# Optimization experiments

Measured on AMD Instinct MI355X. Metric: run time of the kernel, lower is better.

Reference implementation:

```python
import jax, jax.numpy as jnp
import numpy as np

L, E, H, FFE = 4, 512, 8, 512  # layers, embed, heads, ff dim (must equal E for residual)
HD = E // H


def _ln(x, g, b):
    mu = jnp.mean(x, -1, keepdims=True)
    var = jnp.mean((x - mu) ** 2, -1, keepdims=True)
    return (x - mu) / jnp.sqrt(var + 1e-5) * g + b


def setup_inputs() -> dict:
    key = jax.random.key(0)
    ks = jax.random.split(key, 8)
    B, S = 8, 128
    w = lambda k, shape: jax.random.normal(k, shape, jnp.float32) * 0.02
    return {
        "x": jax.random.normal(ks[0], (B, S, E), jnp.float32),
        "Wq": w(ks[1], (L, E, E)), "bq": jnp.zeros((L, E), jnp.float32),
        "Wk": w(ks[2], (L, E, E)), "bk": jnp.zeros((L, E), jnp.float32),
        "Wv": w(ks[3], (L, E, E)), "bv": jnp.zeros((L, E), jnp.float32),
        "Wo": w(ks[4], (L, E, E)), "bo": jnp.zeros((L, E), jnp.float32),
        "Wf": w(ks[5], (L, E, FFE)), "bf": jnp.zeros((L, FFE), jnp.float32),
        "g1": jnp.ones((L, E), jnp.float32), "b1": jnp.zeros((L, E), jnp.float32),
        "g2": jnp.ones((L, FFE), jnp.float32), "b2": jnp.zeros((L, FFE), jnp.float32),
    }


def reference(x, Wq, bq, Wk, bk, Wv, bv, Wo, bo, Wf, bf, g1, b1, g2, b2):
    B, S, _ = x.shape

    def stack(xb, mask):
        # xb: [B,S,E]; mask: [S] bool, True = key position inside current prefix.
        # Non-causal MHA restricted to prefix keys exactly reproduces running
        # the original stack on x[:, :s, :] (query positions beyond the prefix
        # produce values we never read).
        h = xb
        for l in range(L):
            q = (h @ Wq[l] + bq[l]).reshape(B, S, H, HD)
            k = (h @ Wk[l] + bk[l]).reshape(B, S, H, HD)
            v = (h @ Wv[l] + bv[l]).reshape(B, S, H, HD)
            sc = jnp.einsum('bqhd,bkhd->bhqk', q, k) / jnp.sqrt(jnp.float32(HD))
            sc = jnp.where(mask[None, None, None, :], sc, jnp.float32(-1e9))
            a = jax.nn.softmax(sc, axis=-1)
            o = jnp.einsum('bhqk,bkhd->bqhd', a, v).reshape(B, S, E)
            h = _ln(o @ Wo[l] + bo[l] + h, g1[l], b1[l])          # MHA + residual + LN1
            h = _ln(jax.nn.relu(h @ Wf[l] + bf[l]) + h, g2[l], b2[l])  # FF + ReLU + residual + LN2
        return h

    # masks[s-1] selects keys 0..s-1 -> prefix of length s
    masks = jnp.tril(jnp.ones((S, S), bool))
    outs = jax.vmap(stack, in_axes=(None, 0))(x, masks)  # [S, B, S, E]
    idx = jnp.arange(S)
    last = outs[idx, :, idx]  # [S, B, E]: last valid token of each prefix run
    return jnp.transpose(last, (1, 0, 2))  # [B, S, E]
```

## Files before the change

kernel.cpp:

```cpp
#include <hip/hip_runtime.h>
#include <stdint.h>

typedef unsigned short u16;
typedef __attribute__((ext_vector_type(8))) short bf16x8;
typedef __attribute__((ext_vector_type(4))) float f32x4;

#define EE 512
#define NH 8
#define HDm 64
#define SS 128
#define NB 8
#define NL 4
#define QKVW 1536

__device__ __forceinline__ float bf2f(u16 v){ union{uint32_t u; float f;} c; c.u=((uint32_t)v)<<16; return c.f; }
__device__ __forceinline__ u16 f2bf(float f){ union{float f; uint32_t u;} c; c.f=f; uint32_t u=c.u; return (u16)((u + 0x7FFFu + ((u>>16)&1u))>>16); }

__device__ __forceinline__ f32x4 mfma16(bf16x8 a, bf16x8 b, f32x4 c){
  return __builtin_amdgcn_mfma_f32_16x16x32_bf16(a,b,c,0,0,0);
}

__device__ __forceinline__ void gload16(const u16* g, u16* l){
  auto gp = reinterpret_cast<const __attribute__((address_space(1))) uint32_t*>(reinterpret_cast<uintptr_t>(g));
  auto lp = reinterpret_cast<__attribute__((address_space(3))) uint32_t*>(reinterpret_cast<uintptr_t>(l));
  __builtin_amdgcn_global_load_lds(gp, lp, 16, 0, 0);
}

#define ABAR() asm volatile("s_barrier" ::: "memory")
#define SB0()  __builtin_amdgcn_sched_barrier(0)

__device__ __forceinline__ void run_map(int bid, int cb, int U, int& r, int& u){
  int rr = 0;
  for (;;){
    int g = (cb + rr) >> 4;
    int gend = ((g + 1) << 4) - cb;
    int upr = (g + 1) * U;
    int span = (gend - rr) * upr;
    if (bid < span){ r = rr + bid / upr; u = bid % upr; return; }
    bid -= span; rr = gend;
  }
}

__global__ __launch_bounds__(256) void wtransT(const float* __restrict__ W, u16* __restrict__ dst,
                                               int dstL, int dstOff){
  __shared__ float tl[32][33];
  int l = blockIdx.y;
  int tile = blockIdx.x;
  int ot = tile & 15, it = tile >> 4;
  int t = threadIdx.x;
  int c = t & 31, r = t >> 5;
  #pragma unroll
  for (int k=0;k<4;k++){
    int ri = it*32 + r + k*8;
    tl[c][r + k*8] = W[(size_t)l*262144 + (size_t)ri*512 + ot*32 + c];
  }
  __syncthreads();
  #pragma unroll
  for (int k=0;k<4;k++){
    int ro = ot*32 + r + k*8;
    dst[(size_t)l*dstL + (size_t)(dstOff + ro)*512 + it*32 + c] = f2bf(tl[r + k*8][c]);
  }
}

__global__ __launch_bounds__(256) void bfuse(const float* __restrict__ bq, const float* __restrict__ bk,
                                             const float* __restrict__ bv, float* __restrict__ bqkv){
  int i = blockIdx.x*256 + threadIdx.x;
  int l = i / QKVW, n = i % QKVW;
  const float* b = (n < 512) ? bq : ((n < 1024) ? bk : bv);
  bqkv[i] = b[l*EE + (n & 511)];
}

__global__ __launch_bounds__(256) void hinit(const float* __restrict__ x, u16* __restrict__ h0){
  int i = (blockIdx.x*256 + threadIdx.x)*8;
  int e = i & 511;
  int pb = i >> 9;
  int b = pb & 7, pp = pb >> 3;
  const float* xp = x + (((size_t)b*SS + pp)<<9) + e;
  union{ bf16x8 v; u16 u[8]; } r;
  #pragma unroll
  for (int j=0;j<8;j++) r.u[j] = f2bf(xp[j]);
  *(bf16x8*)(h0 + i) = r.v;
}

template<int MODE>
__global__ __launch_bounds__(256) void gemm_bt(const u16* __restrict__ A, const u16* __restrict__ Bt,
                                               const float* __restrict__ bias, const u16* __restrict__ res,
                                               u16* __restrict__ o0, u16* __restrict__ o1, u16* __restrict__ o2,
                                               int cb, size_t res_mask){
  __shared__ u16 As[2][128*32];
  __shared__ u16 Bs[2][128*32];
  int t = threadIdx.x;
  size_t m0;
  if (cb < 0){
    m0 = (size_t)blockIdx.x * 128;
  } else {
    int r, tile; run_map(blockIdx.x, cb, 1, r, tile);
    m0 = (size_t)r*1024 + (size_t)tile*128;
  }
  int n0 = blockIdx.y*128;
  int wid=t>>6, lane=t&63;
  int wm=wid>>1, wn=wid&1, lr=lane&15, lk=(lane>>4)*8;
  f32x4 acc[4][4] = {};
  int srow=t>>2, scol=(t&3)*8;
  const u16* gA = A + (m0+(size_t)srow)*EE + scol;
  const u16* gB = Bt + ((size_t)(n0+srow))*EE + scol;

  auto stage = [&](int kt, int slot){
    int k0 = kt*32;
    u16* lA = As[slot] + t*8;
    u16* lB = Bs[slot] + t*8;
    gload16(gA+k0, lA);
    gload16(gA+64*EE+k0, lA+2048);
    gload16(gB+k0, lB);
    gload16(gB+64*EE+k0, lB+2048);
  };

  stage(0,0); stage(1,1);

  #pragma unroll
  for (int kt=0; kt<16; kt++){
    int slot = kt & 1;
    if (kt < 15) asm volatile("s_waitcnt vmcnt(4)" ::: "memory");
    else         asm volatile("s_waitcnt vmcnt(0)" ::: "memory");
    ABAR();
    bf16x8 a[4], b[4];
    #pragma unroll
    for (int mi=0;mi<4;mi++) a[mi] = *(const bf16x8*)(As[slot] + (wm*64+mi*16+lr)*32 + lk);
    #pragma unroll
    for (int ni=0;ni<4;ni++) b[ni] = *(const bf16x8*)(Bs[slot] + (wn*64+ni*16+lr)*32 + lk);
    asm volatile("s_waitcnt lgkmcnt(0)" ::: "memory");
    SB0();
    ABAR();
    if (kt < 14) stage(kt+2, slot);
    #pragma unroll
    for (int mi=0;mi<4;mi++)
      #pragma unroll
      for (int ni=0;ni<4;ni++)
        acc[mi][ni] = mfma16(a[mi], b[ni], acc[mi][ni]);
  }

  int g4 = lane>>4;
  u16* outp;
  int nb;
  if (MODE==0){ int sel = n0 >> 9; outp = sel==0 ? o0 : (sel==1 ? o1 : o2); nb = n0 & 511; }
  else        { outp = o0; nb = n0; }
  #pragma unroll
  for (int ni=0;ni<4;ni++){
    int coln = wn*64 + ni*16 + lr;
    float bv = bias[n0 + coln];
    int col = nb + coln;
    #pragma unroll
    for (int mi=0;mi<4;mi++){
      #pragma unroll
      for (int j=0;j<4;j++){
        size_t row = m0 + (size_t)(wm*64 + mi*16 + g4*4 + j);
        float v = acc[mi][ni][j] + bv;
        if (MODE==2) v = fmaxf(v, 0.f);
        if (MODE>=1) v += bf2f(res[(row & res_mask)*EE + col]);
        outp[row*EE + col] = f2bf(v);
      }
    }
  }
}

__global__ __launch_bounds__(256) void attn(const u16* __restrict__ Q, const u16* __restrict__ K,
                                            const u16* __restrict__ V, u16* __restrict__ Oq,
                                            int cb, int shared_qkv){
  __shared__ u16 Ks[128*72];
  __shared__ u16 Vt[64*136];
  __shared__ u16 Ps[4][16*136];
  int t = threadIdx.x;
  int idx = blockIdx.x;
  int hh = idx & 7, b = (idx>>3)&7, r = idx>>6;
  int m_run = cb + r;
  const size_t RS = (size_t)SS*NB*EE;
  size_t rbase = shared_qkv ? 0 : (size_t)r*RS;
  size_t hb = (size_t)b*EE + hh*HDm;
  size_t obase = (size_t)r*RS + hb;
  int nkc = m_run/32 + 1;
  int nkt = nkc*2;
  int nqt = m_run/16 + 1;
  int nkr = nkt*16;
  for (int i=t; i<nkr*8; i+=256){
    int row=i>>3, c=(i&7)*8;
    *(uint4*)(Ks + row*72 + c) = *(const uint4*)(K + rbase + (size_t)row*NB*EE + hb + c);
  }
  for (int i=t; i<nkr*8; i+=256){
    int row=i>>3, c=(i&7)*8;
    uint4 raw = *(const uint4*)(V + rbase + (size_t)row*NB*EE + hb + c);
    const u16* pv = (const u16*)&raw;
    #pragma unroll
    for (int j=0;j<8;j++) Vt[(c+j)*136 + row] = pv[j];
  }
  __syncthreads();
  int wid=t>>6, lane=t&63, lr=lane&15, g=lane>>4, lk=(lane>>4)*8;
  u16* Pw = Ps[wid];
  for (int iq=0; iq<2; iq++){
    int qt = wid*2 + iq;
    if (qt >= nqt) continue;
    const u16* qrow = Q + rbase + (size_t)(qt*16+lr)*NB*EE + hb;
    bf16x8 qa0 = *(const bf16x8*)(qrow + lk);
    bf16x8 qa1 = *(const bf16x8*)(qrow + 32 + lk);
    f32x4 sc[8];
    #pragma unroll
    for (int kt=0;kt<8;kt++){
      if (kt < nkt){
        f32x4 c = {};
        bf16x8 kb0 = *(const bf16x8*)(Ks + (kt*16+lr)*72 + lk);
        bf16x8 kb1 = *(const bf16x8*)(Ks + (kt*16+lr)*72 + 32 + lk);
        c = mfma16(qa0, kb0, c);
        c = mfma16(qa1, kb1, c);
        int key = kt*16 + lr;
        #pragma unroll
        for (int i2=0;i2<4;i2++)
          sc[kt][i2] = (key <= m_run) ? c[i2]*0.125f : -1e9f;
      }
    }
    #pragma unroll
    for (int i2=0;i2<4;i2++){
      float v = -3.0e38f;
      #pragma unroll
      for (int kt=0;kt<8;kt++) if (kt<nkt) v = fmaxf(v, sc[kt][i2]);
      v = fmaxf(v, __shfl_xor(v,1));
      v = fmaxf(v, __shfl_xor(v,2));
      v = fmaxf(v, __shfl_xor(v,4));
      v = fmaxf(v, __shfl_xor(v,8));
      float s = 0.f;
      #pragma unroll
      for (int kt=0;kt<8;kt++) if (kt<nkt){ float e2=__expf(sc[kt][i2]-v); sc[kt][i2]=e2; s+=e2; }
      s += __shfl_xor(s,1); s += __shfl_xor(s,2); s += __shfl_xor(s,4); s += __shfl_xor(s,8);
      float inv = 1.f/s;
      #pragma unroll
      for (int kt=0;kt<8;kt++) if (kt<nkt) sc[kt][i2] *= inv;
    }
    #pragma unroll
    for (int kt=0;kt<8;kt++) if (kt<nkt){
      #pragma unroll
      for (int i2=0;i2<4;i2++)
        Pw[(g*4+i2)*136 + kt*16 + lr] = f2bf(sc[kt][i2]);
    }
    f32x4 oa[4] = {};
    #pragma unroll
    for (int kc=0;kc<4;kc++) if (kc<nkc){
      bf16x8 pa = *(const bf16x8*)(Pw + lr*136 + kc*32 + lk);
      #pragma unroll
      for (int dt=0;dt<4;dt++){
        bf16x8 vb = *(const bf16x8*)(Vt + (dt*16+lr)*136 + kc*32 + lk);
        oa[dt] = mfma16(pa, vb, oa[dt]);
      }
    }
    #pragma unroll
    for (int dt=0;dt<4;dt++){
      #pragma unroll
      for (int j=0;j<4;j++){
        size_t prow = (size_t)(qt*16 + g*4 + j);
        Oq[obase + prow*NB*EE + dt*16 + lr] = f2bf(oa[dt][j]);
      }
    }
  }
}

__global__ __launch_bounds__(256) void lnorm(const u16* __restrict__ in, const float* __restrict__ gg,
                                             const float* __restrict__ bb, u16* __restrict__ outp, int cb){
  int r, u; run_map(blockIdx.x, cb, 32, r, u);
  size_t row = (size_t)r*1024 + (size_t)u*4 + (threadIdx.x>>6);
  int lane = threadIdx.x & 63;
  const u16* p = in + row*EE + lane*8;
  union{ bf16x8 v; u16 u[8]; } d; d.v = *(const bf16x8*)p;
  float f[8]; float s=0.f;
  #pragma unroll
  for (int j=0;j<8;j++){ f[j]=bf2f(d.u[j]); s+=f[j]; }
  #pragma unroll
  for (int o=1;o<64;o<<=1) s += __shfl_xor(s,o);
  float mu = s*(1.f/512.f);
  float s2=0.f;
  #pragma unroll
  for (int j=0;j<8;j++){ float tt=f[j]-mu; s2+=tt*tt; }
  #pragma unroll
  for (int o=1;o<64;o<<=1) s2 += __shfl_xor(s2,o);
  float rstd = rsqrtf(s2*(1.f/512.f)+1e-5f);
  union{ bf16x8 v; u16 u[8]; } rr;
  #pragma unroll
  for (int j=0;j<8;j++) rr.u[j] = f2bf((f[j]-mu)*rstd*gg[lane*8+j] + bb[lane*8+j]);
  *(bf16x8*)(outp + row*EE + lane*8) = rr.v;
}

__global__ __launch_bounds__(256) void extract(const u16* __restrict__ h, float* __restrict__ out, int cb){
  int i = blockIdx.x*256 + threadIdx.x;
  int e = i & 511;
  int b = (i >> 9) & 7;
  int r = i >> 12;
  int m = cb + r;
  out[((size_t)b*SS + m)*EE + e] = bf2f(h[(((size_t)r*SS + m)*NB + b)*EE + e]);
}

extern "C" void kernel_launch(void* const* d_in, const int* in_sizes, int n_in,
                              void* d_out, int out_size, void* d_ws, size_t ws_size,
                              hipStream_t stream){
  const float* x   = (const float*)d_in[0];
  const float* Wq  = (const float*)d_in[1];
  const float* bq  = (const float*)d_in[2];
  const float* Wk  = (const float*)d_in[3];
  const float* bk  = (const float*)d_in[4];
  const float* Wv  = (const float*)d_in[5];
  const float* bv  = (const float*)d_in[6];
  const float* Wo  = (const float*)d_in[7];
  const float* bo  = (const float*)d_in[8];
  const float* Wf  = (const float*)d_in[9];
  const float* bfb = (const float*)d_in[10];
  const float* g1  = (const float*)d_in[11];
  const float* b1  = (const float*)d_in[12];
  const float* g2  = (const float*)d_in[13];
  const float* b2  = (const float*)d_in[14];
  float* out = (float*)d_out;

  uint8_t* p = (uint8_t*)d_ws;
  u16* WqkvT = (u16*)p; p += (size_t)NL*QKVW*EE*2;
  u16* WoT   = (u16*)p; p += (size_t)NL*EE*EE*2;
  u16* WfT   = (u16*)p; p += (size_t)NL*EE*EE*2;
  float* bqkv= (float*)p; p += (size_t)NL*QKVW*4;
  u16* h0    = (u16*)p; p += (size_t)SS*NB*EE*2;
  u16* q0    = (u16*)p; p += (size_t)SS*NB*EE*2;
  u16* k0    = (u16*)p; p += (size_t)SS*NB*EE*2;
  u16* v0    = (u16*)p; p += (size_t)SS*NB*EE*2;
  size_t used = (size_t)(p - (uint8_t*)d_ws);

  int RC = 128;
  const size_t PER_RUN = (size_t)SS*NB*EE*2*5;
  while (RC > 1 && used + (size_t)RC*PER_RUN > ws_size) RC >>= 1;

  const size_t BUF = (size_t)RC*SS*NB*EE*2;
  u16* h   = (u16*)p; p += BUF;
  u16* q   = (u16*)p; p += BUF;
  u16* k   = (u16*)p; p += BUF;
  u16* v   = (u16*)p; p += BUF;
  u16* tmp = (u16*)p; p += BUF;

  const size_t NOMASK = ~(size_t)0;
  const int QL = QKVW*EE;
  const int OL = EE*EE;

  wtransT<<<dim3(256,NL),256,0,stream>>>(Wq, WqkvT, QL, 0);
  wtransT<<<dim3(256,NL),256,0,stream>>>(Wk, WqkvT, QL, 512);
  wtransT<<<dim3(256,NL),256,0,stream>>>(Wv, WqkvT, QL, 1024);
  wtransT<<<dim3(256,NL),256,0,stream>>>(Wo, WoT, OL, 0);
  wtransT<<<dim3(256,NL),256,0,stream>>>(Wf, WfT, OL, 0);
  bfuse<<<24,256,0,stream>>>(bq, bk, bv, bqkv);
  hinit<<<256,256,0,stream>>>(x, h0);
  gemm_bt<0><<<dim3(8,12),256,0,stream>>>(h0, WqkvT, bqkv, nullptr, q0, k0, v0, -1, 0);

  for (int cb=0; cb<SS; cb+=RC){
    int t128 = 0;
    for (int r2=0;r2<RC;r2++) t128 += (cb+r2)/16 + 1;

    attn<<<dim3(RC*64),256,0,stream>>>(q0, k0, v0, q, cb, 1);
    gemm_bt<1><<<dim3(t128,4),256,0,stream>>>(q, WoT, bo, h0, tmp, tmp, tmp, cb, (size_t)1023);
    lnorm<<<dim3(t128*32),256,0,stream>>>(tmp, g1, b1, h, cb);
    gemm_bt<2><<<dim3(t128,4),256,0,stream>>>(h, WfT, bfb, h, tmp, tmp, tmp, cb, NOMASK);
    lnorm<<<dim3(t128*32),256,0,stream>>>(tmp, g2, b2, h, cb);

    for (int l=1;l<NL;l++){
      gemm_bt<0><<<dim3(t128,12),256,0,stream>>>(h, WqkvT+(size_t)l*QL, bqkv+l*QKVW, nullptr, q, k, v, cb, 0);
      attn<<<dim3(RC*64),256,0,stream>>>(q, k, v, q, cb, 0);
      gemm_bt<1><<<dim3(t128,4),256,0,stream>>>(q, WoT+(size_t)l*OL, bo+l*EE, h, tmp, tmp, tmp, cb, NOMASK);
      lnorm<<<dim3(t128*32),256,0,stream>>>(tmp, g1+l*EE, b1+l*EE, h, cb);
      gemm_bt<2><<<dim3(t128,4),256,0,stream>>>(h, WfT+(size_t)l*OL, bfb+l*EE, h, tmp, tmp, tmp, cb, NOMASK);
      lnorm<<<dim3(t128*32),256,0,stream>>>(tmp, g2+l*EE, b2+l*EE, h, cb);
    }
    extract<<<dim3(RC*16),256,0,stream>>>(h, out, cb);
  }
}
```

Measured before the change: 1.976 ms.

## Double GEMM K-tile to 64 with XOR-swizzled LDS layout, halve run chunk

```diff
diff --git a/kernel.cpp b/kernel.cpp
--- a/kernel.cpp
+++ b/kernel.cpp
@@ -87,8 +87,8 @@
                                                const float* __restrict__ bias, const u16* __restrict__ res,
                                                u16* __restrict__ o0, u16* __restrict__ o1, u16* __restrict__ o2,
                                                int cb, size_t res_mask){
-  __shared__ u16 As[2][128*32];
-  __shared__ u16 Bs[2][128*32];
+  __shared__ u16 As[2][128*64];
+  __shared__ u16 Bs[2][128*64];
   int t = threadIdx.x;
   size_t m0;
   if (cb < 0){
@@ -99,44 +99,62 @@
   }
   int n0 = blockIdx.y*128;
   int wid=t>>6, lane=t&63;
-  int wm=wid>>1, wn=wid&1, lr=lane&15, lk=(lane>>4)*8;
+  int wm=wid>>1, wn=wid&1, lr=lane&15, lq=lane>>4;
   f32x4 acc[4][4] = {};
-  int srow=t>>2, scol=(t&3)*8;
-  const u16* gA = A + (m0+(size_t)srow)*EE + scol;
-  const u16* gB = Bt + ((size_t)(n0+srow))*EE + scol;
+  int srow = t>>3;
+  int cg = (t&7) ^ (srow&7);
+  const u16* gA = A + (m0+(size_t)srow)*EE + cg*8;
+  const u16* gB = Bt + ((size_t)(n0+srow))*EE + cg*8;
 
   auto stage = [&](int kt, int slot){
-    int k0 = kt*32;
+    int k0 = kt*64;
     u16* lA = As[slot] + t*8;
     u16* lB = Bs[slot] + t*8;
-    gload16(gA+k0, lA);
-    gload16(gA+64*EE+k0, lA+2048);
-    gload16(gB+k0, lB);
-    gload16(gB+64*EE+k0, lB+2048);
+    #pragma unroll
+    for (int j=0;j<4;j++){
+      gload16(gA + (size_t)j*32*EE + k0, lA + j*2048);
+      gload16(gB + (size_t)j*32*EE + k0, lB + j*2048);
+    }
   };
 
   stage(0,0); stage(1,1);
 
   #pragma unroll
-  for (int kt=0; kt<16; kt++){
+  for (int kt=0; kt<8; kt++){
     int slot = kt & 1;
-    if (kt < 15) asm volatile("s_waitcnt vmcnt(4)" ::: "memory");
-    else         asm volatile("s_waitcnt vmcnt(0)" ::: "memory");
+    if (kt < 7) asm volatile("s_waitcnt vmcnt(8)" ::: "memory");
+    else        asm volatile("s_waitcnt vmcnt(0)" ::: "memory");
     ABAR();
-    bf16x8 a[4], b[4];
-    #pragma unroll
-    for (int mi=0;mi<4;mi++) a[mi] = *(const bf16x8*)(As[slot] + (wm*64+mi*16+lr)*32 + lk);
-    #pragma unroll
-    for (int ni=0;ni<4;ni++) b[ni] = *(const bf16x8*)(Bs[slot] + (wn*64+ni*16+lr)*32 + lk);
+    bf16x8 a[4][2], b[4][2];
+    #pragma unroll
+    for (int mi=0;mi<4;mi++){
+      int row = wm*64 + mi*16 + lr;
+      #pragma unroll
+      for (int kk=0;kk<2;kk++){
+        int c = (kk*4 + lq) ^ (row&7);
+        a[mi][kk] = *(const bf16x8*)(As[slot] + row*64 + c*8);
+      }
+    }
+    #pragma unroll
+    for (int ni=0;ni<4;ni++){
+      int row = wn*64 + ni*16 + lr;
+      #pragma unroll
+      for (int kk=0;kk<2;kk++){
+        int c = (kk*4 + lq) ^ (row&7);
+        b[ni][kk] = *(const bf16x8*)(Bs[slot] + row*64 + c*8);
+      }
+    }
     asm volatile("s_waitcnt lgkmcnt(0)" ::: "memory");
     SB0();
     ABAR();
-    if (kt < 14) stage(kt+2, slot);
+    if (kt < 6) stage(kt+2, slot);
     #pragma unroll
     for (int mi=0;mi<4;mi++)
       #pragma unroll
-      for (int ni=0;ni<4;ni++)
-        acc[mi][ni] = mfma16(a[mi], b[ni], acc[mi][ni]);
+      for (int ni=0;ni<4;ni++){
+        acc[mi][ni] = mfma16(a[mi][0], b[ni][0], acc[mi][ni]);
+        acc[mi][ni] = mfma16(a[mi][1], b[ni][1], acc[mi][ni]);
+      }
   }
 
   int g4 = lane>>4;
@@ -325,7 +343,7 @@
   u16* v0    = (u16*)p; p += (size_t)SS*NB*EE*2;
   size_t used = (size_t)(p - (uint8_t*)d_ws);
 
-  int RC = 128;
+  int RC = 64;
   const size_t PER_RUN = (size_t)SS*NB*EE*2*5;
   while (RC > 1 && used + (size_t)RC*PER_RUN > ws_size) RC >>= 1;
 
```

After: 1.945 ms. About the same (-1.6%).

## Fold LayerNorm into GEMM epilogues via row statistics and pre-scaled weights

Applied to the files above, without the earlier changes.

```diff
diff --git a/kernel.cpp b/kernel.cpp
--- a/kernel.cpp
+++ b/kernel.cpp
@@ -42,7 +42,7 @@
 }
 
 __global__ __launch_bounds__(256) void wtransT(const float* __restrict__ W, u16* __restrict__ dst,
-                                               int dstL, int dstOff){
+                                               int dstL, int dstOff, const float* __restrict__ sv, int smode){
   __shared__ float tl[32][33];
   int l = blockIdx.y;
   int tile = blockIdx.x;
@@ -55,10 +55,13 @@
     tl[c][r + k*8] = W[(size_t)l*262144 + (size_t)ri*512 + ot*32 + c];
   }
   __syncthreads();
+  float sc = 1.f;
+  if (smode == 1) sc = sv[l*512 + it*32 + c];
+  else if (smode == 2) sc = (l == 0) ? 1.f : sv[(l-1)*512 + it*32 + c];
   #pragma unroll
   for (int k=0;k<4;k++){
     int ro = ot*32 + r + k*8;
-    dst[(size_t)l*dstL + (size_t)(dstOff + ro)*512 + it*32 + c] = f2bf(tl[r + k*8][c]);
+    dst[(size_t)l*dstL + (size_t)(dstOff + ro)*512 + it*32 + c] = f2bf(tl[r + k*8][c] * sc);
   }
 }
 
@@ -68,6 +71,29 @@
   int l = i / QKVW, n = i % QKVW;
   const float* b = (n < 512) ? bq : ((n < 1024) ? bk : bv);
   bqkv[i] = b[l*EE + (n & 511)];
+}
+
+__global__ __launch_bounds__(256) void gbcomp(const u16* __restrict__ WT, long wtStrideL, int wtOff,
+                                              const float* __restrict__ Wf, const float* __restrict__ bvv,
+                                              int lw0, int lg0, int Lcount,
+                                              float2* __restrict__ outGB, int outStrideL, int outOff){
+  int cidx = blockIdx.x*4 + (threadIdx.x>>6);
+  if (cidx >= Lcount*512) return;
+  int idx = cidx>>9, n = cidx&511;
+  int lane = threadIdx.x & 63;
+  const u16* wt = WT + (size_t)(lw0+idx)*wtStrideL + ((size_t)(wtOff+n))*512 + lane*8;
+  bf16x8 wv = *(const bf16x8*)wt;
+  const float* wsrc = Wf + (size_t)(lw0+idx)*262144 + ((size_t)(lane*8))*512 + n;
+  const float* bp = bvv + (lg0+idx)*512 + lane*8;
+  float gs = 0.f, bs = 0.f;
+  #pragma unroll
+  for (int j=0;j<8;j++){
+    gs += bf2f(((const u16*)&wv)[j]);
+    bs += bp[j]*wsrc[(size_t)j*512];
+  }
+  #pragma unroll
+  for (int o=1;o<64;o<<=1){ gs += __shfl_xor(gs,o); bs += __shfl_xor(bs,o); }
+  if (lane == 0) outGB[idx*outStrideL + outOff + n] = make_float2(gs, bs);
 }
 
 __global__ __launch_bounds__(256) void hinit(const float* __restrict__ x, u16* __restrict__ h0){
@@ -82,11 +108,18 @@
   *(bf16x8*)(h0 + i) = r.v;
 }
 
-template<int MODE>
-__global__ __launch_bounds__(256) void gemm_bt(const u16* __restrict__ A, const u16* __restrict__ Bt,
-                                               const float* __restrict__ bias, const u16* __restrict__ res,
-                                               u16* __restrict__ o0, u16* __restrict__ o1, u16* __restrict__ o2,
-                                               int cb, size_t res_mask){
+template<int EPI, int RESMODE>
+__global__ __launch_bounds__(256) void gemm_bt(const u16* A, const u16* Bt,
+                                               const float* __restrict__ bias,
+                                               const float2* __restrict__ GB,
+                                               const float2* statsA,
+                                               const u16* resb,
+                                               const float2* statsR,
+                                               const float* __restrict__ resG, const float* __restrict__ resB,
+                                               size_t res_mask,
+                                               u16* o0, u16* o1, u16* o2,
+                                               float2* statsOut,
+                                               int cb){
   __shared__ u16 As[2][128*32];
   __shared__ u16 Bs[2][128*32];
   int t = threadIdx.x;
@@ -140,25 +173,89 @@
   }
 
   int g4 = lane>>4;
-  u16* outp;
-  int nb;
-  if (MODE==0){ int sel = n0 >> 9; outp = sel==0 ? o0 : (sel==1 ? o1 : o2); nb = n0 & 511; }
-  else        { outp = o0; nb = n0; }
+  float mu_[4][4] = {}, rs_[4][4] = {};
+  if (EPI==0 || EPI==2 || (EPI==1 && RESMODE==1)){
+    const float2* stp = (EPI==1) ? statsR : statsA;
+    #pragma unroll
+    for (int mi=0;mi<4;mi++){
+      #pragma unroll
+      for (int j=0;j<4;j++){
+        size_t row = m0 + (size_t)(wm*64 + mi*16 + g4*4 + j);
+        float s=0.f, qq=0.f;
+        #pragma unroll
+        for (int k2=0;k2<8;k2++){ float2 e = stp[row*8 + k2]; s += e.x; qq += e.y; }
+        float mu = s*(1.f/512.f);
+        float var = qq*(1.f/512.f) - mu*mu;
+        mu_[mi][j] = mu;
+        rs_[mi][j] = rsqrtf(var + 1e-5f);
+      }
+    }
+  }
+  f32x4 psum[4] = {}, psq[4] = {};
+  u16* outp; int nb;
+  if (EPI==0 || EPI==3){ int sel = n0 >> 9; outp = sel==0 ? o0 : (sel==1 ? o1 : o2); nb = n0 & 511; }
+  else                 { outp = o0; nb = n0; }
   #pragma unroll
   for (int ni=0;ni<4;ni++){
     int coln = wn*64 + ni*16 + lr;
-    float bv = bias[n0 + coln];
-    int col = nb + coln;
+    int gcol = n0 + coln;
+    int col  = nb + coln;
+    float bv = bias[gcol];
+    float gw = 0.f, bw = 0.f, rg = 0.f, rb2 = 0.f;
+    if (EPI==0 || EPI==2){ float2 gbv = GB[(EPI==0) ? gcol : col]; gw = gbv.x; bw = gbv.y; }
+    if ((EPI==1 && RESMODE==1) || EPI==2){ rg = resG[col]; rb2 = resB[col]; }
     #pragma unroll
     for (int mi=0;mi<4;mi++){
       #pragma unroll
       for (int j=0;j<4;j++){
         size_t row = m0 + (size_t)(wm*64 + mi*16 + g4*4 + j);
-        float v = acc[mi][ni][j] + bv;
-        if (MODE==2) v = fmaxf(v, 0.f);
-        if (MODE>=1) v += bf2f(res[(row & res_mask)*EE + col]);
+        float sacc = acc[mi][ni][j];
+        float v;
+        if (EPI==3){
+          v = sacc + bv;
+        } else if (EPI==0){
+          float mu = mu_[mi][j], rs = rs_[mi][j];
+          v = rs*sacc - mu*rs*gw + bw + bv;
+        } else if (EPI==1){
+          float rv;
+          if (RESMODE==0) rv = bf2f(resb[(row & res_mask)*EE + col]);
+          else {
+            float mu = mu_[mi][j], rs = rs_[mi][j];
+            rv = (bf2f(resb[row*EE + col]) - mu)*rs*rg + rb2;
+          }
+          v = sacc + bv + rv;
+        } else {
+          float mu = mu_[mi][j], rs = rs_[mi][j];
+          float u = rs*sacc - mu*rs*gw + bw + bv;
+          u = fmaxf(u, 0.f);
+          float rv = (bf2f(resb[row*EE + col]) - mu)*rs*rg + rb2;
+          v = u + rv;
+        }
         outp[row*EE + col] = f2bf(v);
+        if (EPI==1 || EPI==2){ psum[mi][j] += v; psq[mi][j] += v*v; }
       }
+    }
+  }
+  if (EPI==1 || EPI==2){
+    #pragma unroll
+    for (int o=1;o<16;o<<=1){
+      #pragma unroll
+      for (int mi=0;mi<4;mi++)
+        #pragma unroll
+        for (int j=0;j<4;j++){
+          psum[mi][j] += __shfl_xor(psum[mi][j], o);
+          psq[mi][j]  += __shfl_xor(psq[mi][j], o);
+        }
+    }
+    if (lr == 0){
+      int slot = blockIdx.y*2 + wn;
+      #pragma unroll
+      for (int mi=0;mi<4;mi++)
+        #pragma unroll
+        for (int j=0;j<4;j++){
+          size_t row = m0 + (size_t)(wm*64 + mi*16 + g4*4 + j);
+          statsOut[row*8 + slot] = make_float2(psum[mi][j], psq[mi][j]);
+        }
     }
   }
 }
@@ -260,38 +357,31 @@
   }
 }
 
-__global__ __launch_bounds__(256) void lnorm(const u16* __restrict__ in, const float* __restrict__ gg,
-                                             const float* __restrict__ bb, u16* __restrict__ outp, int cb){
-  int r, u; run_map(blockIdx.x, cb, 32, r, u);
-  size_t row = (size_t)r*1024 + (size_t)u*4 + (threadIdx.x>>6);
-  int lane = threadIdx.x & 63;
-  const u16* p = in + row*EE + lane*8;
-  union{ bf16x8 v; u16 u[8]; } d; d.v = *(const bf16x8*)p;
-  float f[8]; float s=0.f;
-  #pragma unroll
-  for (int j=0;j<8;j++){ f[j]=bf2f(d.u[j]); s+=f[j]; }
-  #pragma unroll
-  for (int o=1;o<64;o<<=1) s += __shfl_xor(s,o);
-  float mu = s*(1.f/512.f);
-  float s2=0.f;
-  #pragma unroll
-  for (int j=0;j<8;j++){ float tt=f[j]-mu; s2+=tt*tt; }
-  #pragma unroll
-  for (int o=1;o<64;o<<=1) s2 += __shfl_xor(s2,o);
-  float rstd = rsqrtf(s2*(1.f/512.f)+1e-5f);
-  union{ bf16x8 v; u16 u[8]; } rr;
-  #pragma unroll
-  for (int j=0;j<8;j++) rr.u[j] = f2bf((f[j]-mu)*rstd*gg[lane*8+j] + bb[lane*8+j]);
-  *(bf16x8*)(outp + row*EE + lane*8) = rr.v;
-}
-
-__global__ __launch_bounds__(256) void extract(const u16* __restrict__ h, float* __restrict__ out, int cb){
-  int i = blockIdx.x*256 + threadIdx.x;
-  int e = i & 511;
-  int b = (i >> 9) & 7;
-  int r = i >> 12;
+__global__ __launch_bounds__(256) void extractLN(const u16* __restrict__ hr2, const float2* __restrict__ stats2,
+                                                 const float* __restrict__ g, const float* __restrict__ b,
+                                                 float* __restrict__ out, int cb){
+  int r = blockIdx.x;
+  int t = threadIdx.x;
   int m = cb + r;
-  out[((size_t)b*SS + m)*EE + e] = bf2f(h[(((size_t)r*SS + m)*NB + b)*EE + e]);
+  #pragma unroll
+  for (int it=0; it<2; it++){
+    int chunk = it*256 + t;
+    int b3 = chunk >> 6;
+    int e0 = (chunk & 63)*8;
+    size_t row = ((size_t)r*SS + m)*NB + b3;
+    float s=0.f, qq=0.f;
+    #pragma unroll
+    for (int k2=0;k2<8;k2++){ float2 e = stats2[row*8 + k2]; s += e.x; qq += e.y; }
+    float mu = s*(1.f/512.f);
+    float var = qq*(1.f/512.f) - mu*mu;
+    float rs = rsqrtf(var + 1e-5f);
+    bf16x8 hv = *(const bf16x8*)(hr2 + row*EE + e0);
+    #pragma unroll
+    for (int j2=0;j2<8;j2++){
+      float v = (bf2f(((const u16*)&hv)[j2]) - mu)*rs*g[e0+j2] + b[e0+j2];
+      out[((size_t)b3*SS + m)*EE + e0 + j2] = v;
+    }
+  }
 }
 
 extern "C" void kernel_launch(void* const* d_in, const int* in_sizes, int n_in,
@@ -315,58 +405,76 @@
   float* out = (float*)d_out;
 
   uint8_t* p = (uint8_t*)d_ws;
-  u16* WqkvT = (u16*)p; p += (size_t)NL*QKVW*EE*2;
-  u16* WoT   = (u16*)p; p += (size_t)NL*EE*EE*2;
-  u16* WfT   = (u16*)p; p += (size_t)NL*EE*EE*2;
-  float* bqkv= (float*)p; p += (size_t)NL*QKVW*4;
-  u16* h0    = (u16*)p; p += (size_t)SS*NB*EE*2;
-  u16* q0    = (u16*)p; p += (size_t)SS*NB*EE*2;
-  u16* k0    = (u16*)p; p += (size_t)SS*NB*EE*2;
-  u16* v0    = (u16*)p; p += (size_t)SS*NB*EE*2;
+  u16* WqkvT  = (u16*)p; p += (size_t)NL*QKVW*EE*2;
+  u16* WoT    = (u16*)p; p += (size_t)NL*EE*EE*2;
+  u16* WfT    = (u16*)p; p += (size_t)NL*EE*EE*2;
+  float* bqkv = (float*)p; p += (size_t)NL*QKVW*4;
+  float2* GBqkv = (float2*)p; p += (size_t)3*QKVW*8;
+  float2* GBf   = (float2*)p; p += (size_t)NL*EE*8;
+  u16* h0 = (u16*)p; p += (size_t)SS*NB*EE*2;
+  u16* q0 = (u16*)p; p += (size_t)SS*NB*EE*2;
+  u16* k0 = (u16*)p; p += (size_t)SS*NB*EE*2;
+  u16* v0 = (u16*)p; p += (size_t)SS*NB*EE*2;
   size_t used = (size_t)(p - (uint8_t*)d_ws);
 
   int RC = 128;
-  const size_t PER_RUN = (size_t)SS*NB*EE*2*5;
+  const size_t PER_RUN = (size_t)SS*NB*EE*2*5 + (size_t)SS*NB*8*8*2;
   while (RC > 1 && used + (size_t)RC*PER_RUN > ws_size) RC >>= 1;
 
   const size_t BUF = (size_t)RC*SS*NB*EE*2;
-  u16* h   = (u16*)p; p += BUF;
+  u16* hr1 = (u16*)p; p += BUF;
+  u16* hr2 = (u16*)p; p += BUF;
   u16* q   = (u16*)p; p += BUF;
   u16* k   = (u16*)p; p += BUF;
   u16* v   = (u16*)p; p += BUF;
-  u16* tmp = (u16*)p; p += BUF;
+  float2* stats1 = (float2*)p; p += (size_t)RC*SS*NB*8*8;
+  float2* stats2 = (float2*)p; p += (size_t)RC*SS*NB*8*8;
 
   const size_t NOMASK = ~(size_t)0;
   const int QL = QKVW*EE;
   const int OL = EE*EE;
 
-  wtransT<<<dim3(256,NL),256,0,stream>>>(Wq, WqkvT, QL, 0);
-  wtransT<<<dim3(256,NL),256,0,stream>>>(Wk, WqkvT, QL, 512);
-  wtransT<<<dim3(256,NL),256,0,stream>>>(Wv, WqkvT, QL, 1024);
-  wtransT<<<dim3(256,NL),256,0,stream>>>(Wo, WoT, OL, 0);
-  wtransT<<<dim3(256,NL),256,0,stream>>>(Wf, WfT, OL, 0);
+  wtransT<<<dim3(256,NL),256,0,stream>>>(Wq, WqkvT, QL, 0,    g2, 2);
+  wtransT<<<dim3(256,NL),256,0,stream>>>(Wk, WqkvT, QL, 512,  g2, 2);
+  wtransT<<<dim3(256,NL),256,0,stream>>>(Wv, WqkvT, QL, 1024, g2, 2);
+  wtransT<<<dim3(256,NL),256,0,stream>>>(Wo, WoT, OL, 0, nullptr, 0);
+  wtransT<<<dim3(256,NL),256,0,stream>>>(Wf, WfT, OL, 0, g1, 1);
   bfuse<<<24,256,0,stream>>>(bq, bk, bv, bqkv);
+  gbcomp<<<384,256,0,stream>>>(WqkvT, QL, 0,    Wq, b2, 1, 0, 3, GBqkv, QKVW, 0);
+  gbcomp<<<384,256,0,stream>>>(WqkvT, QL, 512,  Wk, b2, 1, 0, 3, GBqkv, QKVW, 512);
+  gbcomp<<<384,256,0,stream>>>(WqkvT, QL, 1024, Wv, b2, 1, 0, 3, GBqkv, QKVW, 1024);
+  gbcomp<<<512,256,0,stream>>>(WfT, OL, 0, Wf, b1, 0, 0, 4, GBf, EE, 0);
   hinit<<<256,256,0,stream>>>(x, h0);
-  gemm_bt<0><<<dim3(8,12),256,0,stream>>>(h0, WqkvT, bqkv, nullptr, q0, k0, v0, -1, 0);
+  gemm_bt<3,0><<<dim3(8,12),256,0,stream>>>(h0, WqkvT, bqkv, nullptr, nullptr, nullptr, nullptr,
+                                            nullptr, nullptr, 0, q0, k0, v0, nullptr, -1);
 
   for (int cb=0; cb<SS; cb+=RC){
     int t128 = 0;
     for (int r2=0;r2<RC;r2++) t128 += (cb+r2)/16 + 1;
 
-    attn<<<dim3(RC*64),256,0,stream>>>(q0, k0, v0, q, cb, 1);
-    gemm_bt<1><<<dim3(t128,4),256,0,stream>>>(q, WoT, bo, h0, tmp, tmp, tmp, cb, (size_t)1023);
-    lnorm<<<dim3(t128*32),256,0,stream>>>(tmp, g1, b1, h, cb);
-    gemm_bt<2><<<dim3(t128,4),256,0,stream>>>(h, WfT, bfb, h, tmp, tmp, tmp, cb, NOMASK);
-    lnorm<<<dim3(t128*32),256,0,stream>>>(tmp, g2, b2, h, cb);
-
-    for (int l=1;l<NL;l++){
-      gemm_bt<0><<<dim3(t128,12),256,0,stream>>>(h, WqkvT+(size_t)l*QL, bqkv+l*QKVW, nullptr, q, k, v, cb, 0);
-      attn<<<dim3(RC*64),256,0,stream>>>(q, k, v, q, cb, 0);
-      gemm_bt<1><<<dim3(t128,4),256,0,stream>>>(q, WoT+(size_t)l*OL, bo+l*EE, h, tmp, tmp, tmp, cb, NOMASK);
-      lnorm<<<dim3(t128*32),256,0,stream>>>(tmp, g1+l*EE, b1+l*EE, h, cb);
-      gemm_bt<2><<<dim3(t128,4),256,0,stream>>>(h, WfT+(size_t)l*OL, bfb+l*EE, h, tmp, tmp, tmp, cb, NOMASK);
-      lnorm<<<dim3(t128*32),256,0,stream>>>(tmp, g2+l*EE, b2+l*EE, h, cb);
-    }
-    extract<<<dim3(RC*16),256,0,stream>>>(h, out, cb);
-  }
-}
+    for (int l=0;l<NL;l++){
+      if (l == 0) attn<<<dim3(RC*64),256,0,stream>>>(q0, k0, v0, q, cb, 1);
+      else        attn<<<dim3(RC*64),256,0,stream>>>(q, k, v, q, cb, 0);
+
+      if (l == 0)
+        gemm_bt<1,0><<<dim3(t128,4),256,0,stream>>>(q, WoT, bo, nullptr, nullptr,
+                                                    h0, nullptr, nullptr, nullptr, (size_t)1023,
+                                                    hr1, nullptr, nullptr, stats1, cb);
+      else
+        gemm_bt<1,1><<<dim3(t128,4),256,0,stream>>>(q, WoT+(size_t)l*OL, bo+l*EE, nullptr, nullptr,
+                                                    hr2, stats2, g2+(l-1)*EE, b2+(l-1)*EE, NOMASK,
+                                                    hr1, nullptr, nullptr, stats1, cb);
+
+      gemm_bt<2,1><<<dim3(t128,4),256,0,stream>>>(hr1, WfT+(size_t)l*OL, bfb+l*EE, GBf+l*EE, stats1,
+                                                  hr1, nullptr, g1+l*EE, b1+l*EE, NOMASK,
+                                                  hr2, nullptr, nullptr, stats2, cb);
+
+      if (l < NL-1)
+        gemm_bt<0,0><<<dim3(t128,12),256,0,stream>>>(hr2, WqkvT+(size_t)(l+1)*QL, bqkv+(l+1)*QKVW,
+                                                     GBqkv+(size_t)l*QKVW, stats2,
+                                                     nullptr, nullptr, nullptr, nullptr, 0,
+                                                     q, k, v, nullptr, cb);
+    }
+    extractLN<<<dim3(RC),256,0,stream>>>(hr2, stats2, g2+(NL-1)*EE, b2+(NL-1)*EE, out, cb);
+  }
+}
```

Measured after the change: 3.114 ms. +57.6%, slower.
